# Performance work log

Hardware: AMD Instinct MI355X
Metric: run time of the kernel (lower is better)

Reference implementation:

```python
import jax, jax.numpy as jnp
import numpy as np

B, TD, TE, H, D, V = 64, 256, 256, 512, 256, 50000

def setup_inputs() -> dict:
    key = jax.random.key(0)
    ks = jax.random.split(key, 8)
    return {
        "enc_outputs": jax.random.normal(ks[0], (B, TE, H), jnp.float32),
        "dec_inputs": jax.random.randint(ks[1], (B, TD), 0, V, jnp.int32),
        "state_h": jax.random.normal(ks[2], (B, H), jnp.float32),
        "state_c": jax.random.normal(ks[3], (B, H), jnp.float32),
        "E": jax.random.normal(ks[4], (V, D), jnp.float32) * 0.02,
        "W": jax.random.normal(ks[5], (D, 4 * H), jnp.float32) * 0.02,
        "U": jax.random.normal(ks[6], (H, 4 * H), jnp.float32) * 0.02,
        "b": jnp.zeros((4 * H,), jnp.float32),
    }


def _masked_lstm(x, mask, h0, c0, W, U, b):
    """Keras-semantics masked LSTM: at masked steps states AND outputs are
    carried from the previous step. Gate order i, f, g(cell), o."""
    def step(carry, inp):
        h, c = carry
        xt, mt = inp  # xt: [B,D], mt: [B]
        z = xt @ W + h @ U + b  # [B,4H]
        i, f, g, o = jnp.split(z, 4, axis=-1)
        c_new = jax.nn.sigmoid(f) * c + jax.nn.sigmoid(i) * jnp.tanh(g)
        h_new = jax.nn.sigmoid(o) * jnp.tanh(c_new)
        m = mt[:, None]
        h2 = jnp.where(m, h_new, h)
        c2 = jnp.where(m, c_new, c)
        return (h2, c2), h2
    xs = (jnp.swapaxes(x, 0, 1), jnp.swapaxes(mask, 0, 1))  # time-major
    (hT, cT), hs = jax.lax.scan(step, (h0, c0), xs)
    return jnp.swapaxes(hs, 0, 1), hT, cT  # [B,Td,H]


def reference(enc_outputs, dec_inputs, state_h, state_c, E, W, U, b):
    mask = dec_inputs != 0  # mask_zero=True on Embedding
    x = E[dec_inputs]  # [B,Td,D]
    dec_outputs, hT, cT = _masked_lstm(x, mask, state_h, state_c, W, U, b)
    # Keras Attention (Luong dot, no scale): query=dec_outputs, key=value=enc_outputs
    scores = jnp.einsum('bqh,bkh->bqk', dec_outputs, enc_outputs)
    probs = jax.nn.softmax(scores, axis=-1)
    ctx = jnp.einsum('bqk,bkh->bqh', probs, enc_outputs)
    # query mask propagated from embedding zeroes masked query rows
    ctx = jnp.where(mask[..., None], ctx, 0.0)
    return (ctx, hT, cT)
```

## Files before the change

### kernel.cpp

```cpp
#include <hip/hip_runtime.h>
#include <stdint.h>

typedef __attribute__((ext_vector_type(4))) float f32x4;
typedef __attribute__((ext_vector_type(4))) int i32x4;
typedef __attribute__((ext_vector_type(4))) unsigned short u16x4;
typedef __attribute__((ext_vector_type(8))) __bf16 bf16x8;

#define NB 64
#define TD 256
#define TE 256
#define HH 512
#define DD 256
#define FH 2048
#define KT 768
#define LDK 776

#define WS_ENC   0u
#define WS_ENCT  16777216u
#define WS_DEC   33554432u
#define WS_HPING 50331648u
#define WS_CNT   50462720u
#define WS_WT    50528256u
#define WS_XSEQ  53673984u

#define OUT_HT 8388608u
#define OUT_CT 8421376u

__device__ inline unsigned short f2b(float f) {
  union { float f; unsigned u; } x; x.f = f;
  unsigned r = x.u + 0x7FFFu + ((x.u >> 16) & 1u);
  return (unsigned short)(r >> 16);
}
__device__ inline float sigm(float x)   { return 1.0f / (1.0f + __expf(-x)); }
__device__ inline float tanhf_(float x) { return 1.0f - 2.0f / (__expf(2.0f * x) + 1.0f); }

__device__ inline f32x4 mfma_bf16(i32x4 a, i32x4 b, f32x4 c) {
  return __builtin_amdgcn_mfma_f32_16x16x32_bf16(
      __builtin_bit_cast(bf16x8, a), __builtin_bit_cast(bf16x8, b), c, 0, 0, 0);
}

__device__ inline unsigned poll_word(const unsigned* p) {
  unsigned v;
  asm volatile("global_load_dword %0, %1, off sc0 sc1\n\ts_waitcnt vmcnt(0)"
               : "=v"(v) : "v"(p) : "memory");
  return v;
}
__device__ inline i32x4 load4_bypass(const void* p) {
  i32x4 v;
  asm volatile("global_load_dwordx4 %0, %1, off sc0 sc1" : "=v"(v) : "v"(p) : "memory");
  return v;
}
__device__ inline void store4_wt(void* p, i32x4 v) {
  asm volatile("global_store_dwordx4 %0, %1, off sc0 sc1" :: "v"(p), "v"(v) : "memory");
}
__device__ inline void store_u16_wt(unsigned short* p, unsigned v) {
  asm volatile("global_store_short %0, %1, off sc0 sc1" :: "v"(p), "v"(v) : "memory");
}
__device__ inline void vm_drain() {
  asm volatile("s_waitcnt vmcnt(0)" ::: "memory");
}
__device__ inline void lds_fence() {
  asm volatile("s_waitcnt lgkmcnt(0)" ::: "memory");
}

__global__ __launch_bounds__(256) void enc_prep(const float* __restrict__ enc,
                                                unsigned short* __restrict__ enc_bf,
                                                unsigned short* __restrict__ encT_bf) {
  __shared__ float tile[64][65];
  const int bid = blockIdx.x;
  const int b  = bid >> 5;
  const int kt = (bid >> 3) & 3;
  const int ht = bid & 7;
  const int tr = threadIdx.x >> 6;
  const int tc = threadIdx.x & 63;
#pragma unroll
  for (int i = 0; i < 16; ++i) {
    const int ke = i * 4 + tr;
    const float v = enc[((size_t)b * TE + kt * 64 + ke) * HH + ht * 64 + tc];
    enc_bf[((size_t)b * TE + kt * 64 + ke) * HH + ht * 64 + tc] = f2b(v);
    tile[ke][tc] = v;
  }
  __syncthreads();
  const int hr4 = threadIdx.x >> 4;
  const int k4  = (threadIdx.x & 15) * 4;
#pragma unroll
  for (int jr = 0; jr < 4; ++jr) {
    const int hr = jr * 16 + hr4;
    u16x4 p = { f2b(tile[k4 + 0][hr]), f2b(tile[k4 + 1][hr]),
                f2b(tile[k4 + 2][hr]), f2b(tile[k4 + 3][hr]) };
    *(u16x4*)&encT_bf[((size_t)b * HH + ht * 64 + hr) * TE + kt * 64 + k4] = p;
  }
}

__global__ __launch_bounds__(256) void w_prep(const float* __restrict__ W,
                                              const float* __restrict__ U,
                                              unsigned short* __restrict__ wT) {
  __shared__ float tile[64][65];
  const int kt = blockIdx.x >> 5;
  const int ct = blockIdx.x & 31;
  const int tr = threadIdx.x >> 6;
  const int tc = threadIdx.x & 63;
#pragma unroll
  for (int i = 0; i < 16; ++i) {
    const int kr = i * 4 + tr;
    const int k  = kt * 64 + kr;
    const float v = (k < DD) ? W[(size_t)k * FH + ct * 64 + tc]
                             : U[(size_t)(k - DD) * FH + ct * 64 + tc];
    tile[kr][tc] = v;
  }
  __syncthreads();
  const int cr4 = threadIdx.x >> 4;
  const int k4  = (threadIdx.x & 15) * 4;
#pragma unroll
  for (int jr = 0; jr < 4; ++jr) {
    const int cr = jr * 16 + cr4;
    u16x4 p = { f2b(tile[k4 + 0][cr]), f2b(tile[k4 + 1][cr]),
                f2b(tile[k4 + 2][cr]), f2b(tile[k4 + 3][cr]) };
    *(u16x4*)&wT[((size_t)ct * 64 + cr) * KT + kt * 64 + k4] = p;
  }
}

__global__ __launch_bounds__(64) void x_prep(const float* __restrict__ E,
                                             const int* __restrict__ ids,
                                             unsigned short* __restrict__ xseq) {
  const int bid = blockIdx.x;
  const int b = bid >> 8;
  const int t = bid & 255;
  const int lane = threadIdx.x;
  const int id = ids[b * TD + t];
  f32x4 v = *(const f32x4*)(E + (size_t)id * DD + lane * 4);
  u16x4 p = { f2b(v[0]), f2b(v[1]), f2b(v[2]), f2b(v[3]) };
  *(u16x4*)&xseq[((size_t)t * NB + b) * DD + lane * 4] = p;
}

__global__ __launch_bounds__(256) void h0_prep(const float* __restrict__ h0,
                                               unsigned short* __restrict__ h_ping,
                                               unsigned* __restrict__ cnt) {
  const int i = blockIdx.x * 256 + threadIdx.x;
  if (i < NB * HH) h_ping[i] = f2b(h0[i]);
  if (i < 2 * TD) cnt[i] = 0u;
}

__global__ __launch_bounds__(64, 1) void lstm_kernel(
    const unsigned short* __restrict__ xseq, const int* __restrict__ ids,
    const float* __restrict__ h0f, const float* __restrict__ c0f,
    const unsigned short* __restrict__ wT, const float* __restrict__ bias,
    unsigned short* __restrict__ h_ping,
    unsigned short* __restrict__ dec_bf,
    float* __restrict__ out,
    unsigned* __restrict__ cnt)
{
  const int lane = threadIdx.x;
  const int g  = blockIdx.x >> 5;
  const int s  = blockIdx.x & 31;
  const int u0 = s << 4;
  const int lhi = lane >> 4;
  const int llo = lane & 15;

  __shared__ __align__(16) unsigned short wt[64 * LDK];
  __shared__ int ids_l[32][260];
  __shared__ __align__(64) unsigned short hT[32][32];

  {
    const int r = lane;
    const int c = (r >> 4) * 512 + u0 + (r & 15);
    const unsigned short* src = wT + (size_t)c * KT;
#pragma unroll 8
    for (int j = 0; j < 96; ++j)
      *(i32x4*)&wt[r * LDK + j * 8] = *(const i32x4*)(src + j * 8);
  }
  for (int idx = lane; idx < 32 * 256; idx += 64) {
    const int row = idx >> 8, tt = idx & 255;
    ids_l[row][tt] = ids[(g * 32 + row) * TD + tt];
  }
  __syncthreads();

  float bb[4];
#pragma unroll
  for (int gg = 0; gg < 4; ++gg) bb[gg] = bias[gg * 512 + u0 + llo];

  float h_reg[2][4], c_reg[2][4];
#pragma unroll
  for (int mt = 0; mt < 2; ++mt)
#pragma unroll
    for (int r = 0; r < 4; ++r) {
      const int b = g * 32 + mt * 16 + lhi * 4 + r;
      h_reg[mt][r] = h0f[b * HH + u0 + llo];
      c_reg[mt][r] = c0f[b * HH + u0 + llo];
    }

  unsigned short* hp0 = h_ping;
  unsigned short* hp1 = h_ping + NB * HH;

  for (int t = 0; t < TD; ++t) {
    const unsigned short* h_src = (t & 1) ? hp1 : hp0;
    unsigned short*       h_dst = (t & 1) ? hp0 : hp1;

    int mid[2][4];
#pragma unroll
    for (int mt = 0; mt < 2; ++mt)
#pragma unroll
      for (int r = 0; r < 4; ++r) mid[mt][r] = ids_l[mt * 16 + lhi * 4 + r][t];

    const unsigned short* xp = xseq + ((size_t)t * NB + g * 32) * DD;
    i32x4 xf[2][8];
#pragma unroll
    for (int mt = 0; mt < 2; ++mt) {
      const unsigned short* xr = xp + (mt * 16 + llo) * DD + lhi * 8;
#pragma unroll
      for (int kk = 0; kk < 8; ++kk)
        xf[mt][kk] = *(const i32x4*)(xr + kk * 32);
    }

    f32x4 acc[2][4];
#pragma unroll
    for (int mt = 0; mt < 2; ++mt)
#pragma unroll
      for (int gg = 0; gg < 4; ++gg) acc[mt][gg] = (f32x4){0.f, 0.f, 0.f, 0.f};
#pragma unroll
    for (int kk = 0; kk < 8; ++kk) {
      const int ko = kk * 32 + lhi * 8;
#pragma unroll
      for (int gg = 0; gg < 4; ++gg) {
        i32x4 bfr = *(const i32x4*)&wt[(gg * 16 + llo) * LDK + ko];
        acc[0][gg] = mfma_bf16(xf[0][kk], bfr, acc[0][gg]);
        acc[1][gg] = mfma_bf16(xf[1][kk], bfr, acc[1][gg]);
      }
    }

    if (t > 0) {
      const unsigned* c = cnt + (size_t)g * TD + (t - 1);
      while (poll_word(c) < 32u) {  }
    }

    {
      const unsigned short* hb0 = h_src + (size_t)(g * 32 + llo) * HH + lhi * 8;
      const unsigned short* hb1 = hb0 + 16 * HH;
      i32x4 ha0[16], ha1[16];
#pragma unroll
      for (int kk = 0; kk < 16; ++kk) {
        ha0[kk] = load4_bypass(hb0 + kk * 32);
        ha1[kk] = load4_bypass(hb1 + kk * 32);
      }
      vm_drain();
      __builtin_amdgcn_sched_barrier(0);
#pragma unroll
      for (int kk = 0; kk < 16; ++kk) {
        const int ko = DD + kk * 32 + lhi * 8;
#pragma unroll
        for (int gg = 0; gg < 4; ++gg) {
          i32x4 bfr = *(const i32x4*)&wt[(gg * 16 + llo) * LDK + ko];
          acc[0][gg] = mfma_bf16(ha0[kk], bfr, acc[0][gg]);
          acc[1][gg] = mfma_bf16(ha1[kk], bfr, acc[1][gg]);
        }
      }
    }

    unsigned hb_out[2][4];
#pragma unroll
    for (int mt = 0; mt < 2; ++mt) {
#pragma unroll
      for (int r = 0; r < 4; ++r) {
        const float zi = acc[mt][0][r] + bb[0];
        const float zf = acc[mt][1][r] + bb[1];
        const float zg = acc[mt][2][r] + bb[2];
        const float zo = acc[mt][3][r] + bb[3];
        const float cn = sigm(zf) * c_reg[mt][r] + sigm(zi) * tanhf_(zg);
        const float hn = sigm(zo) * tanhf_(cn);
        if (mid[mt][r] != 0) { c_reg[mt][r] = cn; h_reg[mt][r] = hn; }
        const unsigned hb = f2b(h_reg[mt][r]);
        hb_out[mt][r] = hb;
        hT[mt * 16 + lhi * 4 + r][llo] = (unsigned short)hb;
        const int b = g * 32 + mt * 16 + lhi * 4 + r;
        store_u16_wt(&dec_bf[((size_t)b * TD + t) * HH + u0 + llo], hb);
      }
    }

    if (t < TD - 1) {
      lds_fence();
      __builtin_amdgcn_sched_barrier(0);
      const int br = lane >> 1;
      const int half = lane & 1;
      i32x4 hv = *(const i32x4*)&hT[br][half * 8];
      store4_wt(h_dst + (size_t)(g * 32 + br) * HH + u0 + half * 8, hv);
      vm_drain();
      if (lane == 0)
        __hip_atomic_fetch_add(cnt + (size_t)g * TD + t, 1u,
                               __ATOMIC_RELEASE, __HIP_MEMORY_SCOPE_AGENT);
    }
  }

#pragma unroll
  for (int mt = 0; mt < 2; ++mt)
#pragma unroll
    for (int r = 0; r < 4; ++r) {
      const int b = g * 32 + mt * 16 + lhi * 4 + r;
      out[OUT_HT + (size_t)b * HH + u0 + llo] = h_reg[mt][r];
      out[OUT_CT + (size_t)b * HH + u0 + llo] = c_reg[mt][r];
    }
}

__global__ __launch_bounds__(64, 1) void attn_kernel(
    const unsigned short* __restrict__ dec_bf,
    const unsigned short* __restrict__ enc_bf,
    const unsigned short* __restrict__ encT_bf,
    const int* __restrict__ ids,
    float* __restrict__ out)
{
  const int lane = threadIdx.x;
  const int b  = blockIdx.x >> 4;
  const int q0 = (blockIdx.x & 15) << 4;
  const int lhi = lane >> 4, llo = lane & 15;

  __shared__ __align__(16) unsigned short plds[16 * 264];

  i32x4 qf[16];
  const unsigned short* qb = dec_bf + ((size_t)b * TD + q0 + llo) * HH + lhi * 8;
#pragma unroll
  for (int kk = 0; kk < 16; ++kk) qf[kk] = *(const i32x4*)(qb + kk * 32);

  f32x4 sc[16];
#pragma unroll
  for (int ke = 0; ke < 16; ++ke) sc[ke] = (f32x4){0.f, 0.f, 0.f, 0.f};
#pragma unroll
  for (int kk = 0; kk < 16; ++kk) {
    const unsigned short* eb = enc_bf + ((size_t)b * TE + llo) * HH + kk * 32 + lhi * 8;
#pragma unroll
    for (int ke = 0; ke < 16; ++ke)
      sc[ke] = mfma_bf16(qf[kk], *(const i32x4*)(eb + (size_t)ke * 16 * HH), sc[ke]);
  }

  float mx[4], rinv[4];
#pragma unroll
  for (int r = 0; r < 4; ++r) {
    float m = sc[0][r];
#pragma unroll
    for (int ke = 1; ke < 16; ++ke) m = fmaxf(m, sc[ke][r]);
#pragma unroll
    for (int off = 1; off <= 8; off <<= 1) m = fmaxf(m, __shfl_xor(m, off));
    mx[r] = m;
  }
  float sm[4] = {0.f, 0.f, 0.f, 0.f};
#pragma unroll
  for (int ke = 0; ke < 16; ++ke)
#pragma unroll
    for (int r = 0; r < 4; ++r) {
      const float p = __expf(sc[ke][r] - mx[r]);
      sc[ke][r] = p;
      sm[r] += p;
    }
#pragma unroll
  for (int r = 0; r < 4; ++r) {
    float ss = sm[r];
#pragma unroll
    for (int off = 1; off <= 8; off <<= 1) ss += __shfl_xor(ss, off);
    rinv[r] = 1.0f / ss;
  }

#pragma unroll
  for (int ke = 0; ke < 16; ++ke)
#pragma unroll
    for (int r = 0; r < 4; ++r)
      plds[(lhi * 4 + r) * 264 + ke * 16 + llo] = f2b(sc[ke][r]);
  __syncthreads();

  int mq[4];
#pragma unroll
  for (int r = 0; r < 4; ++r) mq[r] = ids[b * TD + q0 + lhi * 4 + r];

  i32x4 pf[8];
#pragma unroll
  for (int k2 = 0; k2 < 8; ++k2)
    pf[k2] = *(const i32x4*)&plds[llo * 264 + k2 * 32 + lhi * 8];

#pragma unroll
  for (int hh = 0; hh < 2; ++hh) {
    f32x4 cacc[16];
#pragma unroll
    for (int hn = 0; hn < 16; ++hn) cacc[hn] = (f32x4){0.f, 0.f, 0.f, 0.f};
#pragma unroll
    for (int k2 = 0; k2 < 8; ++k2) {
      const unsigned short* tb = encT_bf + ((size_t)b * HH + hh * 256 + llo) * TE + k2 * 32 + lhi * 8;
#pragma unroll
      for (int hn = 0; hn < 16; ++hn)
        cacc[hn] = mfma_bf16(pf[k2], *(const i32x4*)(tb + (size_t)hn * 16 * TE), cacc[hn]);
    }
#pragma unroll
    for (int hn = 0; hn < 16; ++hn)
#pragma unroll
      for (int r = 0; r < 4; ++r) {
        const float vv = mq[r] ? cacc[hn][r] * rinv[r] : 0.0f;
        out[((size_t)b * TD + q0 + lhi * 4 + r) * HH + hh * 256 + hn * 16 + llo] = vv;
      }
  }
}

extern "C" void kernel_launch(void* const* d_in, const int* in_sizes, int n_in,
                              void* d_out, int out_size, void* d_ws, size_t ws_size,
                              hipStream_t stream) {
  const float* enc  = (const float*)d_in[0];
  const int*   ids  = (const int*)d_in[1];
  const float* h0   = (const float*)d_in[2];
  const float* c0   = (const float*)d_in[3];
  const float* E    = (const float*)d_in[4];
  const float* W    = (const float*)d_in[5];
  const float* U    = (const float*)d_in[6];
  const float* bias = (const float*)d_in[7];
  float* out = (float*)d_out;
  char* ws = (char*)d_ws;

  unsigned short* enc_bf  = (unsigned short*)(ws + WS_ENC);
  unsigned short* encT_bf = (unsigned short*)(ws + WS_ENCT);
  unsigned short* dec_bf  = (unsigned short*)(ws + WS_DEC);
  unsigned short* h_ping  = (unsigned short*)(ws + WS_HPING);
  unsigned*       cnt     = (unsigned*)(ws + WS_CNT);
  unsigned short* wT      = (unsigned short*)(ws + WS_WT);
  unsigned short* xseq    = (unsigned short*)(ws + WS_XSEQ);

  enc_prep<<<2048, 256, 0, stream>>>(enc, enc_bf, encT_bf);
  w_prep<<<384, 256, 0, stream>>>(W, U, wT);
  x_prep<<<16384, 64, 0, stream>>>(E, ids, xseq);
  h0_prep<<<128, 256, 0, stream>>>(h0, h_ping, cnt);
  lstm_kernel<<<64, 64, 0, stream>>>(xseq, ids, h0, c0, wT, bias, h_ping, dec_bf, out, cnt);
  attn_kernel<<<1024, 64, 0, stream>>>(dec_bf, enc_bf, encT_bf, ids, out);
}
```

Measured before the change: 1.899 ms.

## Process both batch groups per LSTM block, halving persistent block count

The persistent LSTM kernel now launches 32 blocks instead of 64, and each block loops over both 32-row batch groups inside every timestep, reusing its LDS weight slice for both. The ids table shrinks to ushort so that 64 rows fit in LDS. The aim is to interleave the two groups' recurrences, so one group's barrier wait can overlap the other group's compute, and to cut the number of resident blocks taking part in the cross-block sync. The cost is that per-block work per step doubles and runs serially, which may lengthen the critical path of each step. Truncating ids to ushort is safe here only because the vocabulary is 50000, below 65536.

Result: slower. 3.993 ms (+110.3%).

```diff
diff --git a/kernel.cpp b/kernel.cpp
--- a/kernel.cpp
+++ b/kernel.cpp
@@ -151,14 +151,13 @@
     unsigned* __restrict__ cnt)
 {
   const int lane = threadIdx.x;
-  const int g  = blockIdx.x >> 5;
-  const int s  = blockIdx.x & 31;
+  const int s  = blockIdx.x;
   const int u0 = s << 4;
   const int lhi = lane >> 4;
   const int llo = lane & 15;
 
   __shared__ __align__(16) unsigned short wt[64 * LDK];
-  __shared__ int ids_l[32][260];
+  __shared__ unsigned short ids_l[64][264];
   __shared__ __align__(64) unsigned short hT[32][32];
 
   {
@@ -169,9 +168,9 @@
     for (int j = 0; j < 96; ++j)
       *(i32x4*)&wt[r * LDK + j * 8] = *(const i32x4*)(src + j * 8);
   }
-  for (int idx = lane; idx < 32 * 256; idx += 64) {
+  for (int idx = lane; idx < 64 * 256; idx += 64) {
     const int row = idx >> 8, tt = idx & 255;
-    ids_l[row][tt] = ids[(g * 32 + row) * TD + tt];
+    ids_l[row][tt] = (unsigned short)ids[row * TD + tt];
   }
   __syncthreads();
 
@@ -179,15 +178,17 @@
 #pragma unroll
   for (int gg = 0; gg < 4; ++gg) bb[gg] = bias[gg * 512 + u0 + llo];
 
-  float h_reg[2][4], c_reg[2][4];
-#pragma unroll
-  for (int mt = 0; mt < 2; ++mt)
-#pragma unroll
-    for (int r = 0; r < 4; ++r) {
-      const int b = g * 32 + mt * 16 + lhi * 4 + r;
-      h_reg[mt][r] = h0f[b * HH + u0 + llo];
-      c_reg[mt][r] = c0f[b * HH + u0 + llo];
-    }
+  float h_reg[2][2][4], c_reg[2][2][4];
+#pragma unroll
+  for (int gi = 0; gi < 2; ++gi)
+#pragma unroll
+    for (int mt = 0; mt < 2; ++mt)
+#pragma unroll
+      for (int r = 0; r < 4; ++r) {
+        const int b = gi * 32 + mt * 16 + lhi * 4 + r;
+        h_reg[gi][mt][r] = h0f[b * HH + u0 + llo];
+        c_reg[gi][mt][r] = c0f[b * HH + u0 + llo];
+      }
 
   unsigned short* hp0 = h_ping;
   unsigned short* hp1 = h_ping + NB * HH;
@@ -196,108 +197,114 @@
     const unsigned short* h_src = (t & 1) ? hp1 : hp0;
     unsigned short*       h_dst = (t & 1) ? hp0 : hp1;
 
-    int mid[2][4];
-#pragma unroll
-    for (int mt = 0; mt < 2; ++mt)
-#pragma unroll
-      for (int r = 0; r < 4; ++r) mid[mt][r] = ids_l[mt * 16 + lhi * 4 + r][t];
-
-    const unsigned short* xp = xseq + ((size_t)t * NB + g * 32) * DD;
-    i32x4 xf[2][8];
-#pragma unroll
-    for (int mt = 0; mt < 2; ++mt) {
-      const unsigned short* xr = xp + (mt * 16 + llo) * DD + lhi * 8;
-#pragma unroll
-      for (int kk = 0; kk < 8; ++kk)
-        xf[mt][kk] = *(const i32x4*)(xr + kk * 32);
-    }
-
-    f32x4 acc[2][4];
-#pragma unroll
-    for (int mt = 0; mt < 2; ++mt)
-#pragma unroll
-      for (int gg = 0; gg < 4; ++gg) acc[mt][gg] = (f32x4){0.f, 0.f, 0.f, 0.f};
-#pragma unroll
-    for (int kk = 0; kk < 8; ++kk) {
-      const int ko = kk * 32 + lhi * 8;
-#pragma unroll
-      for (int gg = 0; gg < 4; ++gg) {
-        i32x4 bfr = *(const i32x4*)&wt[(gg * 16 + llo) * LDK + ko];
-        acc[0][gg] = mfma_bf16(xf[0][kk], bfr, acc[0][gg]);
-        acc[1][gg] = mfma_bf16(xf[1][kk], bfr, acc[1][gg]);
-      }
-    }
-
-    if (t > 0) {
-      const unsigned* c = cnt + (size_t)g * TD + (t - 1);
-      while (poll_word(c) < 32u) {  }
-    }
-
-    {
-      const unsigned short* hb0 = h_src + (size_t)(g * 32 + llo) * HH + lhi * 8;
-      const unsigned short* hb1 = hb0 + 16 * HH;
-      i32x4 ha0[16], ha1[16];
-#pragma unroll
-      for (int kk = 0; kk < 16; ++kk) {
-        ha0[kk] = load4_bypass(hb0 + kk * 32);
-        ha1[kk] = load4_bypass(hb1 + kk * 32);
-      }
-      vm_drain();
-      __builtin_amdgcn_sched_barrier(0);
-#pragma unroll
-      for (int kk = 0; kk < 16; ++kk) {
-        const int ko = DD + kk * 32 + lhi * 8;
+#pragma unroll
+    for (int gi = 0; gi < 2; ++gi) {
+      int mid[2][4];
+#pragma unroll
+      for (int mt = 0; mt < 2; ++mt)
+#pragma unroll
+        for (int r = 0; r < 4; ++r)
+          mid[mt][r] = ids_l[gi * 32 + mt * 16 + lhi * 4 + r][t];
+
+      const unsigned short* xp = xseq + ((size_t)t * NB + gi * 32) * DD;
+      i32x4 xf[2][8];
+#pragma unroll
+      for (int mt = 0; mt < 2; ++mt) {
+        const unsigned short* xr = xp + (mt * 16 + llo) * DD + lhi * 8;
+#pragma unroll
+        for (int kk = 0; kk < 8; ++kk)
+          xf[mt][kk] = *(const i32x4*)(xr + kk * 32);
+      }
+
+      f32x4 acc[2][4];
+#pragma unroll
+      for (int mt = 0; mt < 2; ++mt)
+#pragma unroll
+        for (int gg = 0; gg < 4; ++gg) acc[mt][gg] = (f32x4){0.f, 0.f, 0.f, 0.f};
+#pragma unroll
+      for (int kk = 0; kk < 8; ++kk) {
+        const int ko = kk * 32 + lhi * 8;
 #pragma unroll
         for (int gg = 0; gg < 4; ++gg) {
           i32x4 bfr = *(const i32x4*)&wt[(gg * 16 + llo) * LDK + ko];
-          acc[0][gg] = mfma_bf16(ha0[kk], bfr, acc[0][gg]);
-          acc[1][gg] = mfma_bf16(ha1[kk], bfr, acc[1][gg]);
+          acc[0][gg] = mfma_bf16(xf[0][kk], bfr, acc[0][gg]);
+          acc[1][gg] = mfma_bf16(xf[1][kk], bfr, acc[1][gg]);
         }
       }
+
+      if (t > 0) {
+        const unsigned* c = cnt + (size_t)gi * TD + (t - 1);
+        while (poll_word(c) < 32u) {  }
+      }
+
+      {
+        const unsigned short* hb0 = h_src + (size_t)(gi * 32 + llo) * HH + lhi * 8;
+        const unsigned short* hb1 = hb0 + 16 * HH;
+        i32x4 ha0[16], ha1[16];
+#pragma unroll
+        for (int kk = 0; kk < 16; ++kk) {
+          ha0[kk] = load4_bypass(hb0 + kk * 32);
+          ha1[kk] = load4_bypass(hb1 + kk * 32);
+        }
+        vm_drain();
+        __builtin_amdgcn_sched_barrier(0);
+#pragma unroll
+        for (int kk = 0; kk < 16; ++kk) {
+          const int ko = DD + kk * 32 + lhi * 8;
+#pragma unroll
+          for (int gg = 0; gg < 4; ++gg) {
+            i32x4 bfr = *(const i32x4*)&wt[(gg * 16 + llo) * LDK + ko];
+            acc[0][gg] = mfma_bf16(ha0[kk], bfr, acc[0][gg]);
+            acc[1][gg] = mfma_bf16(ha1[kk], bfr, acc[1][gg]);
+          }
+        }
+      }
+
+      unsigned hb_out[2][4];
+#pragma unroll
+      for (int mt = 0; mt < 2; ++mt) {
+#pragma unroll
+        for (int r = 0; r < 4; ++r) {
+          const float zi = acc[mt][0][r] + bb[0];
+          const float zf = acc[mt][1][r] + bb[1];
+          const float zg = acc[mt][2][r] + bb[2];
+          const float zo = acc[mt][3][r] + bb[3];
+          const float cn = sigm(zf) * c_reg[gi][mt][r] + sigm(zi) * tanhf_(zg);
+          const float hn = sigm(zo) * tanhf_(cn);
+          if (mid[mt][r] != 0) { c_reg[gi][mt][r] = cn; h_reg[gi][mt][r] = hn; }
+          const unsigned hb = f2b(h_reg[gi][mt][r]);
+          hb_out[mt][r] = hb;
+          hT[mt * 16 + lhi * 4 + r][llo] = (unsigned short)hb;
+          const int b = gi * 32 + mt * 16 + lhi * 4 + r;
+          store_u16_wt(&dec_bf[((size_t)b * TD + t) * HH + u0 + llo], hb);
+        }
+      }
+
+      if (t < TD - 1) {
+        lds_fence();
+        __builtin_amdgcn_sched_barrier(0);
+        const int br = lane >> 1;
+        const int half = lane & 1;
+        i32x4 hv = *(const i32x4*)&hT[br][half * 8];
+        store4_wt(h_dst + (size_t)(gi * 32 + br) * HH + u0 + half * 8, hv);
+        vm_drain();
+        if (lane == 0)
+          __hip_atomic_fetch_add(cnt + (size_t)gi * TD + t, 1u,
+                                 __ATOMIC_RELEASE, __HIP_MEMORY_SCOPE_AGENT);
+      }
     }
-
-    unsigned hb_out[2][4];
-#pragma unroll
-    for (int mt = 0; mt < 2; ++mt) {
+  }
+
+#pragma unroll
+  for (int gi = 0; gi < 2; ++gi)
+#pragma unroll
+    for (int mt = 0; mt < 2; ++mt)
 #pragma unroll
       for (int r = 0; r < 4; ++r) {
-        const float zi = acc[mt][0][r] + bb[0];
-        const float zf = acc[mt][1][r] + bb[1];
-        const float zg = acc[mt][2][r] + bb[2];
-        const float zo = acc[mt][3][r] + bb[3];
-        const float cn = sigm(zf) * c_reg[mt][r] + sigm(zi) * tanhf_(zg);
-        const float hn = sigm(zo) * tanhf_(cn);
-        if (mid[mt][r] != 0) { c_reg[mt][r] = cn; h_reg[mt][r] = hn; }
-        const unsigned hb = f2b(h_reg[mt][r]);
-        hb_out[mt][r] = hb;
-        hT[mt * 16 + lhi * 4 + r][llo] = (unsigned short)hb;
-        const int b = g * 32 + mt * 16 + lhi * 4 + r;
-        store_u16_wt(&dec_bf[((size_t)b * TD + t) * HH + u0 + llo], hb);
-      }
-    }
-
-    if (t < TD - 1) {
-      lds_fence();
-      __builtin_amdgcn_sched_barrier(0);
-      const int br = lane >> 1;
-      const int half = lane & 1;
-      i32x4 hv = *(const i32x4*)&hT[br][half * 8];
-      store4_wt(h_dst + (size_t)(g * 32 + br) * HH + u0 + half * 8, hv);
-      vm_drain();
-      if (lane == 0)
-        __hip_atomic_fetch_add(cnt + (size_t)g * TD + t, 1u,
-                               __ATOMIC_RELEASE, __HIP_MEMORY_SCOPE_AGENT);
-    }
-  }
-
-#pragma unroll
-  for (int mt = 0; mt < 2; ++mt)
-#pragma unroll
-    for (int r = 0; r < 4; ++r) {
-      const int b = g * 32 + mt * 16 + lhi * 4 + r;
-      out[OUT_HT + (size_t)b * HH + u0 + llo] = h_reg[mt][r];
-      out[OUT_CT + (size_t)b * HH + u0 + llo] = c_reg[mt][r];
-    }
+        const int b = gi * 32 + mt * 16 + lhi * 4 + r;
+        out[OUT_HT + (size_t)b * HH + u0 + llo] = h_reg[gi][mt][r];
+        out[OUT_CT + (size_t)b * HH + u0 + llo] = c_reg[gi][mt][r];
+      }
 }
 
 __global__ __launch_bounds__(64, 1) void attn_kernel(
@@ -421,6 +428,6 @@
   w_prep<<<384, 256, 0, stream>>>(W, U, wT);
   x_prep<<<16384, 64, 0, stream>>>(E, ids, xseq);
   h0_prep<<<128, 256, 0, stream>>>(h0, h_ping, cnt);
-  lstm_kernel<<<64, 64, 0, stream>>>(xseq, ids, h0, c0, wT, bias, h_ping, dec_bf, out, cnt);
+  lstm_kernel<<<32, 64, 0, stream>>>(xseq, ids, h0, c0, wT, bias, h_ping, dec_bf, out, cnt);
   attn_kernel<<<1024, 64, 0, stream>>>(dec_bf, enc_bf, encT_bf, ids, out);
 }
```
